# Kernel tuning notes

Hardware: AMD Instinct MI355X
Metric: run time of the kernel (lower is better)

The kernel has to match this reference:

```python
import jax, jax.numpy as jnp
import numpy as np
jax.config.update('jax_enable_x64', True)

T = 524288      # hash table size (2^19)
D = 3           # input_dim
F = 2           # feature_dim
L = 16          # levels
N_MIN, N_MAX = 16, 512
B = 262144      # batch of query points
V = 2 ** D      # voxel corners

_b = np.exp((np.log(N_MAX) - np.log(N_MIN)) / (L - 1))
RESOLUTIONS = jnp.asarray(np.floor(N_MIN * _b ** np.arange(L)).astype(np.int64)).reshape(1, 1, L, 1)
PRIMES = jnp.asarray(np.array([1, 2654435761, 805459861], dtype=np.int64))
_border = np.empty((D, V), dtype=np.int64)
for i in range(D):
    _border[i, :] = np.array(([0] * 2 ** i + [1] * 2 ** i) * 2 ** (D - i - 1), dtype=np.int64)
BORDER_ADDS = jnp.asarray(_border).reshape(1, D, 1, V)


def setup_inputs() -> dict:
    key = jax.random.key(0)
    kx, kt = jax.random.split(key)
    x = jax.random.uniform(kx, (B, D), dtype=jnp.float32)  # coords in [0,1)
    # nn.Embedding init: uniform(-1e-4, 1e-4) per level
    tables = jax.random.uniform(kt, (L, T, F), dtype=jnp.float32, minval=-1e-4, maxval=1e-4)
    return {"x": x, "tables": tables}


def reference(x, tables):
    # scale to each grid resolution: (B, D, L, 1)
    scaled = x[:, :, None, None] * RESOLUTIONS.astype(x.dtype)
    # voxel corner integer coords: (B, D, L, V)
    grid = jnp.floor(scaled).astype(jnp.int64) + BORDER_ADDS
    # NVIDIA fast hash: xor of coord*prime over dims, mod T -> (B, L, V)
    hashed = grid * PRIMES.reshape(1, D, 1, 1)
    idx = jnp.remainder(jnp.bitwise_xor(jnp.bitwise_xor(hashed[:, 0], hashed[:, 1]), hashed[:, 2]), T)
    # gather per-level features: (B, L, V, F)
    feats = tables[jnp.arange(L)[None, :, None], idx]
    # multilinear interpolation weights: prod over dims -> (B, L, V)
    w = jnp.prod(1.0 - jnp.abs(scaled - grid.astype(scaled.dtype)), axis=1)
    # weighted corner sum -> (B, L, F) -> (B, L*F)
    out = jnp.einsum('blv,blvf->blf', w, feats)
    return out.reshape(x.shape[0], L * F)
```

## Files before the change

kernel.cpp:

```cpp
#include <hip/hip_runtime.h>


constexpr int      kT      = 524288;
constexpr unsigned kMask   = kT - 1;
constexpr int      kB      = 262144;
constexpr unsigned kP1     = 2654435761u;
constexpr unsigned kP2     = 805459861u;
constexpr int      kBins   = 4096;
constexpr int      kCap    = 128;
constexpr int      kOvfCap = 65536;
constexpr int      kCoopTot = 413;

typedef float f32x4 __attribute__((ext_vector_type(4)));
typedef float f32x2 __attribute__((ext_vector_type(2)));

__device__ __forceinline__ unsigned morton12(float x0, float x1, float x2) {
    unsigned a = min(15u, (unsigned)(x0 * 16.0f));
    unsigned b = min(15u, (unsigned)(x1 * 16.0f));
    unsigned c = min(15u, (unsigned)(x2 * 16.0f));
    unsigned key = 0;
#pragma unroll
    for (int i = 3; i >= 0; --i)
        key = (key << 3) | (((a >> i) & 1u) << 2) | (((b >> i) & 1u) << 1) | ((c >> i) & 1u);
    return key;
}

__device__ __forceinline__ f32x2 direct_level(const float x0, const float x1, const float x2,
                                              const float res,
                                              const f32x4* __restrict__ tab4) {
    const float s0 = x0 * res, s1 = x1 * res, s2 = x2 * res;
    const float f0 = floorf(s0), f1 = floorf(s1), f2 = floorf(s2);
    const float r0 = s0 - f0, r1 = s1 - f1, r2 = s2 - f2;
    const unsigned c0 = (unsigned)f0;
    const unsigned h1a = (unsigned)f1 * kP1, h1b = h1a + kP1;
    const unsigned h2a = (unsigned)f2 * kP2, h2b = h2a + kP2;
    const float w0a = 1.0f - r0, w1a = 1.0f - r1, w2a = 1.0f - r2;
    float a0 = 0.0f, a1 = 0.0f;
#pragma unroll
    for (int q = 0; q < 4; ++q) {
        const unsigned g = ((q & 1) ? h1b : h1a) ^ ((q & 2) ? h2b : h2a);
        const unsigned i0 = (c0 ^ g) & kMask;
        const unsigned i1 = ((c0 + 1u) ^ g) & kMask;
        const f32x4 A = tab4[i0 >> 1];
        const f32x4 B = tab4[i1 >> 1];
        const float p0x = (i0 & 1) ? A.z : A.x;
        const float p0y = (i0 & 1) ? A.w : A.y;
        const float p1x = (i1 & 1) ? B.z : B.x;
        const float p1y = (i1 & 1) ? B.w : B.y;
        const float wyz = ((q & 1) ? r1 : w1a) * ((q & 2) ? r2 : w2a);
        const float wl = wyz * w0a;
        const float wr = wyz * r0;
        a0 = fmaf(wl, p0x, fmaf(wr, p1x, a0));
        a1 = fmaf(wl, p0y, fmaf(wr, p1y, a1));
    }
    f32x2 r; r.x = a0; r.y = a1;
    return r;
}

__device__ __forceinline__ void hashenc_body(const float x0, const float x1, const float x2,
                                             const f32x4* __restrict__ tab4base,
                                             f32x4* __restrict__ out, const unsigned sid) {
    f32x4 o[8];
    constexpr float kResF[16] = {16, 20, 25, 32, 40, 50, 64, 80,
                                 101, 128, 161, 203, 256, 322, 406, 512};
#pragma unroll
    for (int l = 0; l < 16; ++l) {
        const f32x2 r = direct_level(x0, x1, x2, kResF[l], tab4base + (size_t)l * (kT / 2));
        if (l & 1) { o[l >> 1].z = r.x; o[l >> 1].w = r.y; }
        else       { o[l >> 1].x = r.x; o[l >> 1].y = r.y; }
    }
    f32x4* op = out + (size_t)sid * 8;
#pragma unroll
    for (int k = 0; k < 8; ++k) __builtin_nontemporal_store(o[k], op + k);
}

template <int L, int N, int RES, int OFF>
__device__ __forceinline__ void coop_fill(const unsigned lane,
                                          const unsigned bx, const unsigned by, const unsigned bz,
                                          const f32x2* __restrict__ tab2,
                                          f32x2* __restrict__ wlds) {
    const unsigned lo0 = (bx * RES) >> 4, lo1 = (by * RES) >> 4, lo2 = (bz * RES) >> 4;
    const unsigned h1 = lo1 * kP1, h2 = lo2 * kP2;
    constexpr int NC = N * N * N;
#pragma unroll
    for (int k = 0; k < (NC + 63) / 64; ++k) {
        const int t = (int)lane + 64 * k;
        if (t < NC) {
            const unsigned dx = (unsigned)t / (N * N);
            const unsigned rem = (unsigned)t % (N * N);
            const unsigned dy = rem / N, dz = rem % N;
            const unsigned idx = ((lo0 + dx) ^ (h1 + dy * kP1) ^ (h2 + dz * kP2)) & kMask;
            wlds[OFF + t] = tab2[(size_t)L * kT + idx];
        }
    }
}

template <int N, int RES, int OFF>
__device__ __forceinline__ f32x2 coop_interp(const float x0, const float x1, const float x2,
                                             const unsigned bx, const unsigned by, const unsigned bz,
                                             const f32x2* __restrict__ wlds) {
    const float res = (float)RES;
    const float s0 = x0 * res, s1 = x1 * res, s2 = x2 * res;
    const float f0 = floorf(s0), f1 = floorf(s1), f2 = floorf(s2);
    const float r0 = s0 - f0, r1 = s1 - f1, r2 = s2 - f2;
    const unsigned lo0 = (bx * RES) >> 4, lo1 = (by * RES) >> 4, lo2 = (bz * RES) >> 4;
    const unsigned i0 = min((unsigned)f0 - lo0, (unsigned)(N - 2));
    const unsigned i1 = min((unsigned)f1 - lo1, (unsigned)(N - 2));
    const unsigned i2 = min((unsigned)f2 - lo2, (unsigned)(N - 2));
    const int s00 = OFF + (int)(i0 * (N * N) + i1 * N + i2);
    const f32x2 c000 = wlds[s00],             c001 = wlds[s00 + 1];
    const f32x2 c010 = wlds[s00 + N],         c011 = wlds[s00 + N + 1];
    const f32x2 c100 = wlds[s00 + N * N],     c101 = wlds[s00 + N * N + 1];
    const f32x2 c110 = wlds[s00 + N * N + N], c111 = wlds[s00 + N * N + N + 1];
    const float w0a = 1.f - r0, w1a = 1.f - r1, w2a = 1.f - r2;
    float a0, a1;
    const float w00 = w0a * w1a, w01 = w0a * r1, w10 = r0 * w1a, w11 = r0 * r1;
    a0 = w00 * w2a * c000.x; a1 = w00 * w2a * c000.y;
    a0 = fmaf(w00 * r2, c001.x, a0); a1 = fmaf(w00 * r2, c001.y, a1);
    a0 = fmaf(w01 * w2a, c010.x, a0); a1 = fmaf(w01 * w2a, c010.y, a1);
    a0 = fmaf(w01 * r2, c011.x, a0); a1 = fmaf(w01 * r2, c011.y, a1);
    a0 = fmaf(w10 * w2a, c100.x, a0); a1 = fmaf(w10 * w2a, c100.y, a1);
    a0 = fmaf(w10 * r2, c101.x, a0); a1 = fmaf(w10 * r2, c101.y, a1);
    a0 = fmaf(w11 * w2a, c110.x, a0); a1 = fmaf(w11 * r2 / r2 * r2, 0.f, a1);
    a1 = fmaf(w11 * w2a, c110.y, fmaf(w10 * r2, c101.y, fmaf(w10 * w2a, c100.y,
         fmaf(w01 * r2, c011.y, fmaf(w01 * w2a, c010.y, fmaf(w00 * r2, c001.y, w00 * w2a * c000.y))))));
    a0 = fmaf(w11 * w2a, c110.x, fmaf(w10 * r2, c101.x, fmaf(w10 * w2a, c100.x,
         fmaf(w01 * r2, c011.x, fmaf(w01 * w2a, c010.x, fmaf(w00 * r2, c001.x, w00 * w2a * c000.x))))));
    a0 = fmaf(w11 * r2, c111.x, a0);
    a1 = fmaf(w11 * r2, c111.y, a1);
    f32x2 r; r.x = a0; r.y = a1;
    return r;
}

__global__ __launch_bounds__(256) void scatter_kernel(const float* __restrict__ x,
                                                      unsigned* __restrict__ cnt,
                                                      f32x4* __restrict__ xsort,
                                                      f32x4* __restrict__ ovf) {
    const int i = blockIdx.x * 256 + threadIdx.x;
    const float x0 = x[3 * i], x1 = x[3 * i + 1], x2 = x[3 * i + 2];
    const unsigned key = morton12(x0, x1, x2);
    const unsigned slot = atomicAdd(&cnt[key], 1u);
    f32x4 v;
    v.x = x0; v.y = x1; v.z = x2; v.w = __uint_as_float((unsigned)i);
    if (slot < (unsigned)kCap) {
        xsort[key * kCap + slot] = v;
    } else {
        const unsigned o = atomicAdd(&cnt[kBins], 1u);
        if (o < (unsigned)kOvfCap) ovf[o] = v;
    }
}

__global__ __launch_bounds__(256) void hashenc_sorted(const f32x4* __restrict__ xsort,
                                                      const unsigned* __restrict__ cnt,
                                                      const f32x2* __restrict__ tab2,
                                                      const f32x4* __restrict__ tab4base,
                                                      f32x4* __restrict__ out) {
    __shared__ f32x2 lds[4][kCoopTot];
    const int tid = threadIdx.x;
    const int bid = (int)((blockIdx.x & 7) * 256 + (blockIdx.x >> 3));
    const int gs  = bid * 256 + tid;
    const int bin = gs >> 7;
    const int sl  = gs & (kCap - 1);
    const unsigned n = min(cnt[bin], (unsigned)kCap);
    if ((unsigned)(sl & 64) >= n) return;
    const bool valid = (unsigned)sl < n;
    const f32x4 v = xsort[gs];
    const float x0 = valid ? v.x : 0.5f;
    const float x1 = valid ? v.y : 0.5f;
    const float x2 = valid ? v.z : 0.5f;

    const unsigned key = (unsigned)bin;
    const unsigned bx = ((key >> 2) & 1) | ((key >> 4) & 2) | ((key >> 6) & 4) | ((key >> 8) & 8);
    const unsigned by = ((key >> 1) & 1) | ((key >> 3) & 2) | ((key >> 5) & 4) | ((key >> 7) & 8);
    const unsigned bz = ((key     ) & 1) | ((key >> 2) & 2) | ((key >> 4) & 4) | ((key >> 6) & 8);

    f32x2* wlds = lds[tid >> 6];
    const unsigned lane = (unsigned)(tid & 63);
    coop_fill<0, 2, 16, 0>(lane, bx, by, bz, tab2, wlds);
    coop_fill<1, 4, 20, 8>(lane, bx, by, bz, tab2, wlds);
    coop_fill<2, 4, 25, 72>(lane, bx, by, bz, tab2, wlds);
    coop_fill<3, 3, 32, 136>(lane, bx, by, bz, tab2, wlds);
    coop_fill<4, 5, 40, 163>(lane, bx, by, bz, tab2, wlds);
    coop_fill<6, 5, 64, 288>(lane, bx, by, bz, tab2, wlds);

    f32x4 o[8];
    { const f32x2 r = direct_level(x0, x1, x2, 50.f,  tab4base + (size_t)5  * (kT / 2)); o[2].z = r.x; o[2].w = r.y; }
    { const f32x2 r = direct_level(x0, x1, x2, 80.f,  tab4base + (size_t)7  * (kT / 2)); o[3].z = r.x; o[3].w = r.y; }
    { const f32x2 r = direct_level(x0, x1, x2, 101.f, tab4base + (size_t)8  * (kT / 2)); o[4].x = r.x; o[4].y = r.y; }
    { const f32x2 r = direct_level(x0, x1, x2, 128.f, tab4base + (size_t)9  * (kT / 2)); o[4].z = r.x; o[4].w = r.y; }
    { const f32x2 r = direct_level(x0, x1, x2, 161.f, tab4base + (size_t)10 * (kT / 2)); o[5].x = r.x; o[5].y = r.y; }
    { const f32x2 r = direct_level(x0, x1, x2, 203.f, tab4base + (size_t)11 * (kT / 2)); o[5].z = r.x; o[5].w = r.y; }
    { const f32x2 r = direct_level(x0, x1, x2, 256.f, tab4base + (size_t)12 * (kT / 2)); o[6].x = r.x; o[6].y = r.y; }
    { const f32x2 r = direct_level(x0, x1, x2, 322.f, tab4base + (size_t)13 * (kT / 2)); o[6].z = r.x; o[6].w = r.y; }
    { const f32x2 r = direct_level(x0, x1, x2, 406.f, tab4base + (size_t)14 * (kT / 2)); o[7].x = r.x; o[7].y = r.y; }
    { const f32x2 r = direct_level(x0, x1, x2, 512.f, tab4base + (size_t)15 * (kT / 2)); o[7].z = r.x; o[7].w = r.y; }
    { const f32x2 r = coop_interp<2, 16, 0>(x0, x1, x2, bx, by, bz, wlds);   o[0].x = r.x; o[0].y = r.y; }
    { const f32x2 r = coop_interp<4, 20, 8>(x0, x1, x2, bx, by, bz, wlds);   o[0].z = r.x; o[0].w = r.y; }
    { const f32x2 r = coop_interp<4, 25, 72>(x0, x1, x2, bx, by, bz, wlds);  o[1].x = r.x; o[1].y = r.y; }
    { const f32x2 r = coop_interp<3, 32, 136>(x0, x1, x2, bx, by, bz, wlds); o[1].z = r.x; o[1].w = r.y; }
    { const f32x2 r = coop_interp<5, 40, 163>(x0, x1, x2, bx, by, bz, wlds); o[2].x = r.x; o[2].y = r.y; }
    { const f32x2 r = coop_interp<5, 64, 288>(x0, x1, x2, bx, by, bz, wlds); o[3].x = r.x; o[3].y = r.y; }

    if (valid) {
        f32x4* op = out + (size_t)__float_as_uint(v.w) * 8;
#pragma unroll
        for (int k = 0; k < 8; ++k) __builtin_nontemporal_store(o[k], op + k);
    }
}

__global__ __launch_bounds__(256) void cleanup_kernel(const f32x4* __restrict__ ovf,
                                                      const unsigned* __restrict__ cnt,
                                                      const f32x4* __restrict__ tab4base,
                                                      f32x4* __restrict__ out) {
    const unsigned oc = min(cnt[kBins], (unsigned)kOvfCap);
    for (unsigned j = threadIdx.x; j < oc; j += 256) {
        const f32x4 v = ovf[j];
        hashenc_body(v.x, v.y, v.z, tab4base, out, __float_as_uint(v.w));
    }
}

__global__ __launch_bounds__(256, 4) void hashenc_direct(const float* __restrict__ x,
                                                         const f32x4* __restrict__ tab4base,
                                                         f32x4* __restrict__ out) {
    const int i = blockIdx.x * 256 + threadIdx.x;
    hashenc_body(x[3 * i], x[3 * i + 1], x[3 * i + 2], tab4base, out, (unsigned)i);
}

extern "C" void kernel_launch(void* const* d_in, const int* in_sizes, int n_in,
                              void* d_out, int out_size, void* d_ws, size_t ws_size,
                              hipStream_t stream) {
    const float*  x    = (const float*)d_in[0];
    const f32x2*  tab2 = (const f32x2*)d_in[1];
    const f32x4*  tab4 = (const f32x4*)d_in[1];
    f32x4*        out  = (f32x4*)d_out;

    const size_t cntBytes   = (size_t)(kBins + 16) * 4;
    const size_t ovfBytes   = (size_t)kOvfCap * 16;
    const size_t xsortBytes = (size_t)kBins * kCap * 16;
    const size_t need = cntBytes + ovfBytes + xsortBytes;

    if (ws_size >= need) {
        unsigned* cnt   = (unsigned*)d_ws;
        f32x4*    ovf   = (f32x4*)((char*)d_ws + cntBytes);
        f32x4*    xsort = ovf + kOvfCap;
        hipMemsetAsync(cnt, 0, cntBytes, stream);
        scatter_kernel<<<kB / 256, 256, 0, stream>>>(x, cnt, xsort, ovf);
        hashenc_sorted<<<(kBins * kCap) / 256, 256, 0, stream>>>(xsort, cnt, tab2, tab4, out);
        cleanup_kernel<<<1, 256, 0, stream>>>(ovf, cnt, tab4, out);
    } else {
        hashenc_direct<<<kB / 256, 256, 0, stream>>>(x, tab4, out);
    }
}
```

Before: 155.4 us.

## Split sorted encoder into coarse LDS-cooperative and fine direct-gather kernels

Splits the single sorted encoding kernel into two launches. The coarse kernel now stages levels 0-7 (adding levels 5 and 7 at resolutions 50 and 80) cooperatively in LDS, which roughly doubles the per-wavefront LDS footprint. A separate fine kernel with a higher occupancy bound does direct hashed gathers for levels 8-15. The aim is to lower register pressure and raise occupancy for the gather-heavy levels, and to cut global gathers for the mid levels. The cost is a second pass over the sorted points, one more launch, and less occupancy in the coarse kernel from the larger LDS use. The interpolation code is also cleaned of redundant recomputation.

```diff
diff --git a/kernel.cpp b/kernel.cpp
--- a/kernel.cpp
+++ b/kernel.cpp
@@ -9,7 +9,7 @@
 constexpr int      kBins   = 4096;
 constexpr int      kCap    = 128;
 constexpr int      kOvfCap = 65536;
-constexpr int      kCoopTot = 413;
+constexpr int      kCoopTot = 845;
 
 typedef float f32x4 __attribute__((ext_vector_type(4)));
 typedef float f32x2 __attribute__((ext_vector_type(2)));
@@ -113,21 +113,16 @@
     const f32x2 c100 = wlds[s00 + N * N],     c101 = wlds[s00 + N * N + 1];
     const f32x2 c110 = wlds[s00 + N * N + N], c111 = wlds[s00 + N * N + N + 1];
     const float w0a = 1.f - r0, w1a = 1.f - r1, w2a = 1.f - r2;
-    float a0, a1;
     const float w00 = w0a * w1a, w01 = w0a * r1, w10 = r0 * w1a, w11 = r0 * r1;
-    a0 = w00 * w2a * c000.x; a1 = w00 * w2a * c000.y;
-    a0 = fmaf(w00 * r2, c001.x, a0); a1 = fmaf(w00 * r2, c001.y, a1);
+    float a0 = w00 * w2a * c000.x;
+    float a1 = w00 * w2a * c000.y;
+    a0 = fmaf(w00 * r2,  c001.x, a0); a1 = fmaf(w00 * r2,  c001.y, a1);
     a0 = fmaf(w01 * w2a, c010.x, a0); a1 = fmaf(w01 * w2a, c010.y, a1);
-    a0 = fmaf(w01 * r2, c011.x, a0); a1 = fmaf(w01 * r2, c011.y, a1);
+    a0 = fmaf(w01 * r2,  c011.x, a0); a1 = fmaf(w01 * r2,  c011.y, a1);
     a0 = fmaf(w10 * w2a, c100.x, a0); a1 = fmaf(w10 * w2a, c100.y, a1);
-    a0 = fmaf(w10 * r2, c101.x, a0); a1 = fmaf(w10 * r2, c101.y, a1);
-    a0 = fmaf(w11 * w2a, c110.x, a0); a1 = fmaf(w11 * r2 / r2 * r2, 0.f, a1);
-    a1 = fmaf(w11 * w2a, c110.y, fmaf(w10 * r2, c101.y, fmaf(w10 * w2a, c100.y,
-         fmaf(w01 * r2, c011.y, fmaf(w01 * w2a, c010.y, fmaf(w00 * r2, c001.y, w00 * w2a * c000.y))))));
-    a0 = fmaf(w11 * w2a, c110.x, fmaf(w10 * r2, c101.x, fmaf(w10 * w2a, c100.x,
-         fmaf(w01 * r2, c011.x, fmaf(w01 * w2a, c010.x, fmaf(w00 * r2, c001.x, w00 * w2a * c000.x))))));
-    a0 = fmaf(w11 * r2, c111.x, a0);
-    a1 = fmaf(w11 * r2, c111.y, a1);
+    a0 = fmaf(w10 * r2,  c101.x, a0); a1 = fmaf(w10 * r2,  c101.y, a1);
+    a0 = fmaf(w11 * w2a, c110.x, a0); a1 = fmaf(w11 * w2a, c110.y, a1);
+    a0 = fmaf(w11 * r2,  c111.x, a0); a1 = fmaf(w11 * r2,  c111.y, a1);
     f32x2 r; r.x = a0; r.y = a1;
     return r;
 }
@@ -150,10 +145,9 @@
     }
 }
 
-__global__ __launch_bounds__(256) void hashenc_sorted(const f32x4* __restrict__ xsort,
+__global__ __launch_bounds__(256) void hashenc_coarse(const f32x4* __restrict__ xsort,
                                                       const unsigned* __restrict__ cnt,
                                                       const f32x2* __restrict__ tab2,
-                                                      const f32x4* __restrict__ tab4base,
                                                       f32x4* __restrict__ out) {
     __shared__ f32x2 lds[4][kCoopTot];
     const int tid = threadIdx.x;
@@ -176,36 +170,57 @@
 
     f32x2* wlds = lds[tid >> 6];
     const unsigned lane = (unsigned)(tid & 63);
-    coop_fill<0, 2, 16, 0>(lane, bx, by, bz, tab2, wlds);
-    coop_fill<1, 4, 20, 8>(lane, bx, by, bz, tab2, wlds);
-    coop_fill<2, 4, 25, 72>(lane, bx, by, bz, tab2, wlds);
+    coop_fill<0, 2, 16,   0>(lane, bx, by, bz, tab2, wlds);
+    coop_fill<1, 4, 20,   8>(lane, bx, by, bz, tab2, wlds);
+    coop_fill<2, 4, 25,  72>(lane, bx, by, bz, tab2, wlds);
     coop_fill<3, 3, 32, 136>(lane, bx, by, bz, tab2, wlds);
     coop_fill<4, 5, 40, 163>(lane, bx, by, bz, tab2, wlds);
-    coop_fill<6, 5, 64, 288>(lane, bx, by, bz, tab2, wlds);
-
-    f32x4 o[8];
-    { const f32x2 r = direct_level(x0, x1, x2, 50.f,  tab4base + (size_t)5  * (kT / 2)); o[2].z = r.x; o[2].w = r.y; }
-    { const f32x2 r = direct_level(x0, x1, x2, 80.f,  tab4base + (size_t)7  * (kT / 2)); o[3].z = r.x; o[3].w = r.y; }
-    { const f32x2 r = direct_level(x0, x1, x2, 101.f, tab4base + (size_t)8  * (kT / 2)); o[4].x = r.x; o[4].y = r.y; }
-    { const f32x2 r = direct_level(x0, x1, x2, 128.f, tab4base + (size_t)9  * (kT / 2)); o[4].z = r.x; o[4].w = r.y; }
-    { const f32x2 r = direct_level(x0, x1, x2, 161.f, tab4base + (size_t)10 * (kT / 2)); o[5].x = r.x; o[5].y = r.y; }
-    { const f32x2 r = direct_level(x0, x1, x2, 203.f, tab4base + (size_t)11 * (kT / 2)); o[5].z = r.x; o[5].w = r.y; }
-    { const f32x2 r = direct_level(x0, x1, x2, 256.f, tab4base + (size_t)12 * (kT / 2)); o[6].x = r.x; o[6].y = r.y; }
-    { const f32x2 r = direct_level(x0, x1, x2, 322.f, tab4base + (size_t)13 * (kT / 2)); o[6].z = r.x; o[6].w = r.y; }
-    { const f32x2 r = direct_level(x0, x1, x2, 406.f, tab4base + (size_t)14 * (kT / 2)); o[7].x = r.x; o[7].y = r.y; }
-    { const f32x2 r = direct_level(x0, x1, x2, 512.f, tab4base + (size_t)15 * (kT / 2)); o[7].z = r.x; o[7].w = r.y; }
-    { const f32x2 r = coop_interp<2, 16, 0>(x0, x1, x2, bx, by, bz, wlds);   o[0].x = r.x; o[0].y = r.y; }
-    { const f32x2 r = coop_interp<4, 20, 8>(x0, x1, x2, bx, by, bz, wlds);   o[0].z = r.x; o[0].w = r.y; }
-    { const f32x2 r = coop_interp<4, 25, 72>(x0, x1, x2, bx, by, bz, wlds);  o[1].x = r.x; o[1].y = r.y; }
+    coop_fill<5, 6, 50, 288>(lane, bx, by, bz, tab2, wlds);
+    coop_fill<6, 5, 64, 504>(lane, bx, by, bz, tab2, wlds);
+    coop_fill<7, 6, 80, 629>(lane, bx, by, bz, tab2, wlds);
+
+    f32x4 o[4];
+    { const f32x2 r = coop_interp<2, 16,   0>(x0, x1, x2, bx, by, bz, wlds); o[0].x = r.x; o[0].y = r.y; }
+    { const f32x2 r = coop_interp<4, 20,   8>(x0, x1, x2, bx, by, bz, wlds); o[0].z = r.x; o[0].w = r.y; }
+    { const f32x2 r = coop_interp<4, 25,  72>(x0, x1, x2, bx, by, bz, wlds); o[1].x = r.x; o[1].y = r.y; }
     { const f32x2 r = coop_interp<3, 32, 136>(x0, x1, x2, bx, by, bz, wlds); o[1].z = r.x; o[1].w = r.y; }
     { const f32x2 r = coop_interp<5, 40, 163>(x0, x1, x2, bx, by, bz, wlds); o[2].x = r.x; o[2].y = r.y; }
-    { const f32x2 r = coop_interp<5, 64, 288>(x0, x1, x2, bx, by, bz, wlds); o[3].x = r.x; o[3].y = r.y; }
+    { const f32x2 r = coop_interp<6, 50, 288>(x0, x1, x2, bx, by, bz, wlds); o[2].z = r.x; o[2].w = r.y; }
+    { const f32x2 r = coop_interp<5, 64, 504>(x0, x1, x2, bx, by, bz, wlds); o[3].x = r.x; o[3].y = r.y; }
+    { const f32x2 r = coop_interp<6, 80, 629>(x0, x1, x2, bx, by, bz, wlds); o[3].z = r.x; o[3].w = r.y; }
 
     if (valid) {
         f32x4* op = out + (size_t)__float_as_uint(v.w) * 8;
 #pragma unroll
-        for (int k = 0; k < 8; ++k) __builtin_nontemporal_store(o[k], op + k);
-    }
+        for (int k = 0; k < 4; ++k) __builtin_nontemporal_store(o[k], op + k);
+    }
+}
+
+__global__ __launch_bounds__(256, 4) void hashenc_fine(const f32x4* __restrict__ xsort,
+                                                       const unsigned* __restrict__ cnt,
+                                                       const f32x4* __restrict__ tab4base,
+                                                       f32x4* __restrict__ out) {
+    const int bid = (int)((blockIdx.x & 7) * 256 + (blockIdx.x >> 3));
+    const int gs  = bid * 256 + (int)threadIdx.x;
+    const int bin = gs >> 7;
+    const int sl  = gs & (kCap - 1);
+    const unsigned n = min(cnt[bin], (unsigned)kCap);
+    if ((unsigned)sl >= n) return;
+    const f32x4 v = xsort[gs];
+    const float x0 = v.x, x1 = v.y, x2 = v.z;
+
+    constexpr float kResF[8] = {101, 128, 161, 203, 256, 322, 406, 512};
+    f32x4 o[4];
+#pragma unroll
+    for (int j = 0; j < 8; ++j) {
+        const int l = 8 + j;
+        const f32x2 r = direct_level(x0, x1, x2, kResF[j], tab4base + (size_t)l * (kT / 2));
+        if (j & 1) { o[j >> 1].z = r.x; o[j >> 1].w = r.y; }
+        else       { o[j >> 1].x = r.x; o[j >> 1].y = r.y; }
+    }
+    f32x4* op = out + (size_t)__float_as_uint(v.w) * 8 + 4;
+#pragma unroll
+    for (int k = 0; k < 4; ++k) __builtin_nontemporal_store(o[k], op + k);
 }
 
 __global__ __launch_bounds__(256) void cleanup_kernel(const f32x4* __restrict__ ovf,
@@ -245,7 +260,8 @@
         f32x4*    xsort = ovf + kOvfCap;
         hipMemsetAsync(cnt, 0, cntBytes, stream);
         scatter_kernel<<<kB / 256, 256, 0, stream>>>(x, cnt, xsort, ovf);
-        hashenc_sorted<<<(kBins * kCap) / 256, 256, 0, stream>>>(xsort, cnt, tab2, tab4, out);
+        hashenc_coarse<<<(kBins * kCap) / 256, 256, 0, stream>>>(xsort, cnt, tab2, out);
+        hashenc_fine<<<(kBins * kCap) / 256, 256, 0, stream>>>(xsort, cnt, tab4, out);
         cleanup_kernel<<<1, 256, 0, stream>>>(ovf, cnt, tab4, out);
     } else {
         hashenc_direct<<<kB / 256, 256, 0, stream>>>(x, tab4, out);
```

Result: slower. 164.5 us (+5.9%).
